# Kernel optimization log

Hardware: AMD Instinct MI355X
Metric: run time of the kernel (lower is better)

The kernel has to match this reference:

```python
import jax, jax.numpy as jnp
import numpy as np

# Dims: V = in-simplices, E = out-simplices, K = input_ch, C = target_ch,
#       D = in_depth_ch, O = o_depth_ch
V = 8192
E = 8192
K = 64
C = 64
D = 8
O = 8


def setup_inputs() -> dict:
    key = jax.random.key(0)
    k1, k2, k3, k4 = jax.random.split(key, 4)
    x = jax.random.normal(k1, (V, K, D), dtype=jnp.float32)
    G = jax.random.normal(k2, (E, V), dtype=jnp.float32) * 0.02  # dense boundary operator
    # o_depth_ch stacked TensorLinear weights: W[o, d, k, c], bias b[o, c, d]
    W = jax.random.normal(k3, (O, D, K, C), dtype=jnp.float32) * (1.0 / np.sqrt(K))
    b = jax.random.normal(k4, (O, C, D), dtype=jnp.float32) * 0.02
    return {"x": x, "G": G, "W": W, "b": b}


def reference(x, G, W, b):
    # Per out-depth channel o: y_o[v,c,d] = sum_k x[v,k,d] * W[o,d,k,c] + b[o,c,d]
    # output[e,c,o] = sum_{v,d} G[e,v] * y_o[v,c,d]
    # Fuse: sum over d inside the first contraction; bias contributes
    # rowsum(G)[e] * sum_d b[o,c,d].
    z = jnp.einsum('vkd,odkc->ovc', x, W) + b.sum(axis=-1)[:, None, :]  # [O, V, C]
    out = jnp.einsum('ev,ovc->eco', G, z)                               # [E, C, O]
    return out
```

## Files before the change

### kernel.cpp

```cpp
#include <hip/hip_runtime.h>
#include <hip/hip_bf16.h>

#define V_DIM 8192
#define E_DIM 8192
#define KD    512
#define CO    512

typedef __attribute__((ext_vector_type(8))) short short8;
typedef __attribute__((ext_vector_type(8))) unsigned short ushort8;
typedef __attribute__((ext_vector_type(4))) float f32x4;

__device__ __forceinline__ unsigned short f2b(float f) {
  __hip_bfloat16 h = __float2bfloat16(f);
  return __builtin_bit_cast(unsigned short, h);
}

__device__ __forceinline__ void gload_lds16(const void* g, void* l) {
  __builtin_amdgcn_global_load_lds(
      (const __attribute__((address_space(1))) void*)g,
      (__attribute__((address_space(3))) void*)l, 16, 0, 0);
}

__global__ void convert_x(const float* __restrict__ x, unsigned short* __restrict__ xb) {
  const size_t i = ((size_t)blockIdx.x * 256 + threadIdx.x) * 8;
  float4 f0 = *(const float4*)(x + i);
  float4 f1 = *(const float4*)(x + i + 4);
  ushort8 u;
  u[0]=f2b(f0.x); u[1]=f2b(f0.y); u[2]=f2b(f0.z); u[3]=f2b(f0.w);
  u[4]=f2b(f1.x); u[5]=f2b(f1.y); u[6]=f2b(f1.z); u[7]=f2b(f1.w);
  *(ushort8*)(xb + i) = u;
}

__global__ void repack_w(const float* __restrict__ W, const float* __restrict__ b,
                         float* __restrict__ Wt, float* __restrict__ bsum) {
  const int idx = blockIdx.x * 256 + threadIdx.x;
  const int j = idx >> 9, kd = idx & 511;
  const int c = j >> 3, o = j & 7, k = kd >> 3, d = kd & 7;
  Wt[idx] = W[(((o * 8 + d) * 64 + k) << 6) + c];
  if (idx < 512) {
    const int cc = idx >> 3, oo = idx & 7;
    float s = 0.f;
#pragma unroll
    for (int dd = 0; dd < 8; ++dd) s += b[((oo * 64 + cc) << 3) + dd];
    bsum[idx] = s;
  }
}

template<int NT, bool OUT_BF16, bool HASBIAS, bool SWIZ>
__global__ __launch_bounds__(512, 2)
void gemm_bt(const float* __restrict__ A, const unsigned short* __restrict__ B,
             const float* __restrict__ bias, void* __restrict__ Cout,
             int ldA, int ldB, int ldC) {
  static_assert((NT - 2) % 6 == 0, "pipeline needs (NT-2) divisible by 6");
  __shared__ __align__(16) unsigned short As[2][128 * 64];
  __shared__ __align__(16) unsigned short Bs[3][128 * 64];

  const int tid  = threadIdx.x;
  const int lane = tid & 63;
  const int w    = tid >> 6;
  const int wm   = w >> 2;
  const int wn   = w & 3;

  int bm, bn;
  if (SWIZ) {
    int bid = blockIdx.x + (blockIdx.y << 2);
    bid = ((bid & 7) << 5) | (bid >> 3);
    bm = bid >> 2; bn = bid & 3;
  } else {
    bm = blockIdx.y; bn = blockIdx.x;
  }
  const int m0 = bm * 128, n0 = bn * 128;

  const int sr  = tid >> 3;
  const int sc  = tid & 7;
  const int brl = lane >> 3;
  const int bch = lane & 7;

  const float* agB0 = A + (size_t)(m0 + sr) * ldA + sc * 8;
  const float* agB1 = agB0 + (size_t)64 * ldA;
  const int aw0 = sr * 64 + ((sc ^ (sr & 7)) * 8);
  const int aw1 = aw0 + 64 * 64;

  const unsigned short* bsrc0 =
      B + (size_t)(n0 + w * 8 + brl) * ldB + ((bch ^ brl) * 8);
  const unsigned short* bsrc1 = bsrc0 + (size_t)64 * ldB;
  const int bd0 = (w * 8) * 64;
  const int bd1 = (64 + w * 8) * 64;

  f32x4 acc[4][2];
#pragma unroll
  for (int i = 0; i < 4; ++i)
#pragma unroll
    for (int j = 0; j < 2; ++j) acc[i][j] = (f32x4)0.0f;

  f32x4 pf[2][4];

#define STAGE_LOAD(T, C, BSLOT) do {                                      \
    const int kt_ = (T) << 6;                                             \
    pf[(C)][0] = *(const f32x4*)(agB0 + kt_);                             \
    pf[(C)][1] = *(const f32x4*)(agB0 + kt_ + 4);                         \
    pf[(C)][2] = *(const f32x4*)(agB1 + kt_);                             \
    pf[(C)][3] = *(const f32x4*)(agB1 + kt_ + 4);                         \
    gload_lds16(bsrc0 + kt_, &Bs[(BSLOT)][bd0]);                          \
    gload_lds16(bsrc1 + kt_, &Bs[(BSLOT)][bd1]);                          \
  } while (0)

#define STAGE_WRITE(C, ASLOT) do {                                        \
    ushort8 u0_, u1_;                                                     \
    u0_[0]=f2b(pf[(C)][0][0]); u0_[1]=f2b(pf[(C)][0][1]);                 \
    u0_[2]=f2b(pf[(C)][0][2]); u0_[3]=f2b(pf[(C)][0][3]);                 \
    u0_[4]=f2b(pf[(C)][1][0]); u0_[5]=f2b(pf[(C)][1][1]);                 \
    u0_[6]=f2b(pf[(C)][1][2]); u0_[7]=f2b(pf[(C)][1][3]);                 \
    u1_[0]=f2b(pf[(C)][2][0]); u1_[1]=f2b(pf[(C)][2][1]);                 \
    u1_[2]=f2b(pf[(C)][2][2]); u1_[3]=f2b(pf[(C)][2][3]);                 \
    u1_[4]=f2b(pf[(C)][3][0]); u1_[5]=f2b(pf[(C)][3][1]);                 \
    u1_[6]=f2b(pf[(C)][3][2]); u1_[7]=f2b(pf[(C)][3][3]);                 \
    *(ushort8*)(&As[(ASLOT)][aw0]) = u0_;                                 \
    *(ushort8*)(&As[(ASLOT)][aw1]) = u1_;                                 \
  } while (0)

#define COMPUTE(ASLOT, BSLOT) do {                                        \
    const unsigned short* Ab_ = As[(ASLOT)];                              \
    const unsigned short* Bb_ = Bs[(BSLOT)];                              \
    _Pragma("unroll")                                                     \
    for (int kk = 0; kk < 2; ++kk) {                                      \
      const int ck_ = kk * 4 + (lane >> 4);                               \
      short8 af_[4], bf_[2];                                              \
      _Pragma("unroll")                                                   \
      for (int mi = 0; mi < 4; ++mi) {                                    \
        const int r_ = wm * 64 + mi * 16 + (lane & 15);                   \
        af_[mi] = *(const short8*)(Ab_ + r_ * 64 + ((ck_ ^ (r_ & 7)) * 8)); \
      }                                                                   \
      _Pragma("unroll")                                                   \
      for (int ni = 0; ni < 2; ++ni) {                                    \
        const int r_ = wn * 32 + ni * 16 + (lane & 15);                   \
        bf_[ni] = *(const short8*)(Bb_ + r_ * 64 + ((ck_ ^ (r_ & 7)) * 8)); \
      }                                                                   \
      _Pragma("unroll")                                                   \
      for (int mi = 0; mi < 4; ++mi)                                      \
        _Pragma("unroll")                                                 \
        for (int ni = 0; ni < 2; ++ni)                                    \
          acc[mi][ni] = __builtin_amdgcn_mfma_f32_16x16x32_bf16(          \
              af_[mi], bf_[ni], acc[mi][ni], 0, 0, 0);                    \
    }                                                                     \
  } while (0)

#define BAR() do {                                                        \
    __builtin_amdgcn_sched_barrier(0);                                    \
    __builtin_amdgcn_s_barrier();                                         \
    __builtin_amdgcn_sched_barrier(0);                                    \
  } while (0)

  STAGE_LOAD(0, 0, 0);
  STAGE_LOAD(1, 1, 1);
  asm volatile("s_waitcnt vmcnt(6)" ::: "memory");
  STAGE_WRITE(0, 0);
  asm volatile("s_waitcnt lgkmcnt(0)" ::: "memory");
  BAR();

#pragma unroll 1
  for (int tb = 0; tb < NT - 2; tb += 6) {
#pragma unroll
    for (int jj = 0; jj < 6; ++jj) {
      STAGE_LOAD(tb + jj + 2, jj & 1, (jj + 2) % 3);
      COMPUTE(jj & 1, jj % 3);
      BAR();
      asm volatile("s_waitcnt vmcnt(6)" ::: "memory");
      STAGE_WRITE((jj + 1) & 1, (jj + 1) & 1);
      asm volatile("s_waitcnt lgkmcnt(0)" ::: "memory");
      BAR();
    }
  }

  COMPUTE((NT - 2) & 1, (NT - 2) % 3);
  BAR();
  asm volatile("s_waitcnt vmcnt(0)" ::: "memory");
  STAGE_WRITE((NT - 1) & 1, (NT - 1) & 1);
  asm volatile("s_waitcnt lgkmcnt(0)" ::: "memory");
  BAR();
  COMPUTE((NT - 1) & 1, (NT - 1) % 3);

#undef STAGE_LOAD
#undef STAGE_WRITE
#undef COMPUTE
#undef BAR

  const int rg = lane >> 4;
  const int cl = lane & 15;
#pragma unroll
  for (int mi = 0; mi < 4; ++mi) {
#pragma unroll
    for (int r = 0; r < 4; ++r) {
      const int row = m0 + wm * 64 + mi * 16 + rg * 4 + r;
      float bv = 0.0f;
      if (HASBIAS) bv = bias[row];
#pragma unroll
      for (int ni = 0; ni < 2; ++ni) {
        const int col = n0 + wn * 32 + ni * 16 + cl;
        const float v = acc[mi][ni][r] + bv;
        if (OUT_BF16)
          ((unsigned short*)Cout)[(size_t)row * ldC + col] = f2b(v);
        else
          ((float*)Cout)[(size_t)row * ldC + col] = v;
      }
    }
  }
}

extern "C" void kernel_launch(void* const* d_in, const int* in_sizes, int n_in,
                              void* d_out, int out_size, void* d_ws, size_t ws_size,
                              hipStream_t stream) {
  const float* x = (const float*)d_in[0];
  const float* G = (const float*)d_in[1];
  const float* W = (const float*)d_in[2];
  const float* b = (const float*)d_in[3];

  char* ws = (char*)d_ws;
  unsigned short* xb = (unsigned short*)ws;
  float* Wt          = (float*)(ws + (8u << 20));
  float* bs          = (float*)(ws + (9u << 20));
  unsigned short* Zt = (unsigned short*)(ws + (9u << 20) + (1u << 16));

  hipLaunchKernelGGL(convert_x, dim3(2048), dim3(256), 0, stream, x, xb);
  hipLaunchKernelGGL(repack_w, dim3(1024), dim3(256), 0, stream, W, b, Wt, bs);

  hipLaunchKernelGGL((gemm_bt<8, true, true, false>), dim3(64, 4), dim3(512), 0,
                     stream, Wt, xb, bs, (void*)Zt, KD, KD, V_DIM);

  hipLaunchKernelGGL((gemm_bt<128, false, false, true>), dim3(4, 64), dim3(512), 0,
                     stream, G, Zt, (const float*)nullptr, (void*)d_out,
                     V_DIM, V_DIM, CO);
}
```

Baseline: 474.7 us.

## Split-K the large G GEMM across two slices with atomic accumulation

The second GEMM (G times Z) is split along the V reduction into two halves via blockIdx.z. This doubles the block count from 256 to 512 so each CU can hold two resident blocks. The output is zeroed first by a new kernel, and partial results are combined with float atomicAdd. The pipeline loop gains a remainder path for NT values not divisible by 6, and s_setprio raises wave priority around the MFMA compute phase. The cost is an extra zeroing pass, atomic output traffic, and nondeterministic summation order.

```diff
diff --git a/kernel.cpp b/kernel.cpp
--- a/kernel.cpp
+++ b/kernel.cpp
@@ -46,12 +46,15 @@
   }
 }
 
-template<int NT, bool OUT_BF16, bool HASBIAS, bool SWIZ>
+__global__ void zero_out(float4* __restrict__ p) {
+  p[(size_t)blockIdx.x * 256 + threadIdx.x] = make_float4(0.f, 0.f, 0.f, 0.f);
+}
+
+template<int NT, bool OUT_BF16, bool HASBIAS, bool SWIZ, bool ATOMIC>
 __global__ __launch_bounds__(512, 2)
 void gemm_bt(const float* __restrict__ A, const unsigned short* __restrict__ B,
              const float* __restrict__ bias, void* __restrict__ Cout,
              int ldA, int ldB, int ldC) {
-  static_assert((NT - 2) % 6 == 0, "pipeline needs (NT-2) divisible by 6");
   __shared__ __align__(16) unsigned short As[2][128 * 64];
   __shared__ __align__(16) unsigned short Bs[3][128 * 64];
 
@@ -70,19 +73,20 @@
     bm = blockIdx.y; bn = blockIdx.x;
   }
   const int m0 = bm * 128, n0 = bn * 128;
+  const int koff = blockIdx.z * (NT << 6);
 
   const int sr  = tid >> 3;
   const int sc  = tid & 7;
   const int brl = lane >> 3;
   const int bch = lane & 7;
 
-  const float* agB0 = A + (size_t)(m0 + sr) * ldA + sc * 8;
+  const float* agB0 = A + (size_t)(m0 + sr) * ldA + koff + sc * 8;
   const float* agB1 = agB0 + (size_t)64 * ldA;
   const int aw0 = sr * 64 + ((sc ^ (sr & 7)) * 8);
   const int aw1 = aw0 + 64 * 64;
 
   const unsigned short* bsrc0 =
-      B + (size_t)(n0 + w * 8 + brl) * ldB + ((bch ^ brl) * 8);
+      B + (size_t)(n0 + w * 8 + brl) * ldB + koff + ((bch ^ brl) * 8);
   const unsigned short* bsrc1 = bsrc0 + (size_t)64 * ldB;
   const int bd0 = (w * 8) * 64;
   const int bd1 = (64 + w * 8) * 64;
@@ -151,6 +155,18 @@
     __builtin_amdgcn_sched_barrier(0);                                    \
   } while (0)
 
+#define STEP(T, PA, PA1, PB2) do {                                        \
+    STAGE_LOAD((T) + 2, PA, PB2);                                         \
+    __builtin_amdgcn_s_setprio(1);                                        \
+    COMPUTE(PA, (T) % 3);                                                 \
+    __builtin_amdgcn_s_setprio(0);                                        \
+    BAR();                                                                \
+    asm volatile("s_waitcnt vmcnt(6)" ::: "memory");                      \
+    STAGE_WRITE(PA1, PA1);                                                \
+    asm volatile("s_waitcnt lgkmcnt(0)" ::: "memory");                    \
+    BAR();                                                                \
+  } while (0)
+
   STAGE_LOAD(0, 0, 0);
   STAGE_LOAD(1, 1, 1);
   asm volatile("s_waitcnt vmcnt(6)" ::: "memory");
@@ -158,21 +174,22 @@
   asm volatile("s_waitcnt lgkmcnt(0)" ::: "memory");
   BAR();
 
+  constexpr int NIT  = NT - 2;
+  constexpr int MAIN = (NIT / 6) * 6;
+
 #pragma unroll 1
-  for (int tb = 0; tb < NT - 2; tb += 6) {
-#pragma unroll
-    for (int jj = 0; jj < 6; ++jj) {
-      STAGE_LOAD(tb + jj + 2, jj & 1, (jj + 2) % 3);
-      COMPUTE(jj & 1, jj % 3);
-      BAR();
-      asm volatile("s_waitcnt vmcnt(6)" ::: "memory");
-      STAGE_WRITE((jj + 1) & 1, (jj + 1) & 1);
-      asm volatile("s_waitcnt lgkmcnt(0)" ::: "memory");
-      BAR();
-    }
-  }
-
+  for (int tb = 0; tb < MAIN; tb += 6) {
+#pragma unroll
+    for (int jj = 0; jj < 6; ++jj)
+      STEP(tb + jj, jj & 1, (jj + 1) & 1, (jj + 2) % 3);
+  }
+#pragma unroll
+  for (int jj = 0; jj < NIT - MAIN; ++jj)
+    STEP(MAIN + jj, (MAIN + jj) & 1, (MAIN + jj + 1) & 1, (MAIN + jj + 2) % 3);
+
+  __builtin_amdgcn_s_setprio(1);
   COMPUTE((NT - 2) & 1, (NT - 2) % 3);
+  __builtin_amdgcn_s_setprio(0);
   BAR();
   asm volatile("s_waitcnt vmcnt(0)" ::: "memory");
   STAGE_WRITE((NT - 1) & 1, (NT - 1) & 1);
@@ -184,6 +201,7 @@
 #undef STAGE_WRITE
 #undef COMPUTE
 #undef BAR
+#undef STEP
 
   const int rg = lane >> 4;
   const int cl = lane & 15;
@@ -198,10 +216,13 @@
       for (int ni = 0; ni < 2; ++ni) {
         const int col = n0 + wn * 32 + ni * 16 + cl;
         const float v = acc[mi][ni][r] + bv;
-        if (OUT_BF16)
+        if (OUT_BF16) {
           ((unsigned short*)Cout)[(size_t)row * ldC + col] = f2b(v);
-        else
+        } else if (ATOMIC) {
+          atomicAdd(((float*)Cout) + (size_t)row * ldC + col, v);
+        } else {
           ((float*)Cout)[(size_t)row * ldC + col] = v;
+        }
       }
     }
   }
@@ -224,10 +245,12 @@
   hipLaunchKernelGGL(convert_x, dim3(2048), dim3(256), 0, stream, x, xb);
   hipLaunchKernelGGL(repack_w, dim3(1024), dim3(256), 0, stream, W, b, Wt, bs);
 
-  hipLaunchKernelGGL((gemm_bt<8, true, true, false>), dim3(64, 4), dim3(512), 0,
-                     stream, Wt, xb, bs, (void*)Zt, KD, KD, V_DIM);
-
-  hipLaunchKernelGGL((gemm_bt<128, false, false, true>), dim3(4, 64), dim3(512), 0,
-                     stream, G, Zt, (const float*)nullptr, (void*)d_out,
-                     V_DIM, V_DIM, CO);
-}
+  hipLaunchKernelGGL((gemm_bt<8, true, true, false, false>), dim3(64, 4), dim3(512),
+                     0, stream, Wt, xb, bs, (void*)Zt, KD, KD, V_DIM);
+
+  hipLaunchKernelGGL(zero_out, dim3(4096), dim3(256), 0, stream, (float4*)d_out);
+
+  hipLaunchKernelGGL((gemm_bt<64, false, false, true, true>), dim3(4, 64, 2),
+                     dim3(512), 0, stream, G, Zt, (const float*)nullptr,
+                     (void*)d_out, V_DIM, V_DIM, CO);
+}
```

Measured after the change: 471.3 us. No clear change (-0.7%).
